# Kernel tuning notes

Hardware: AMD Instinct MI355X
Metric: run time of the kernel (lower is better)

The kernel has to match this reference:

```python
import jax, jax.numpy as jnp
import numpy as np

DIM = 384; HEADS = 6; POINTS = 4; LEVELS = 3; HID = 96
B = 2; D0 = 12; H0 = 12; W0 = 12
NMID = D0 * H0 * W0          # mid-level tokens
NTOK = 73 * NMID // 8        # total tokens across 3 scales


def _ln(x, w, b, eps=1e-6):
    m = x.mean(-1, keepdims=True)
    v = ((x - m) ** 2).mean(-1, keepdims=True)
    return (x - m) * jax.lax.rsqrt(v + eps) * w + b


def _make_ref(shapes):
    # matches get_reference_points: per-level normalized centers, stacked as (d, x, y)
    refs = []
    for (D_, H_, W_) in shapes:
        d = (jnp.arange(D_, dtype=jnp.float32) + 0.5) / D_
        y = (jnp.arange(H_, dtype=jnp.float32) + 0.5) / H_
        x = (jnp.arange(W_, dtype=jnp.float32) + 0.5) / W_
        dd, yy, xx = jnp.meshgrid(d, y, x, indexing='ij')
        refs.append(jnp.stack([dd.ravel(), xx.ravel(), yy.ravel()], -1))
    return jnp.concatenate(refs, 0)[None, :, None, :]  # [1, N, 1, 3]


def _sample_level(v, D_, H_, W_, loc):
    # v: [B,S,h,hd]; loc: [B,Nq,h,P,3] normalized (d,x,y); trilinear, zero padding,
    # align_corners=False semantics (pixel = norm*size - 0.5)
    Bq, Nq, h, P, _ = loc.shape
    hd = v.shape[-1]
    pd = loc[..., 0] * D_ - 0.5
    px = loc[..., 1] * W_ - 0.5
    py = loc[..., 2] * H_ - 0.5
    d0 = jnp.floor(pd); x0 = jnp.floor(px); y0 = jnp.floor(py)
    fd = pd - d0; fx = px - x0; fy = py - y0
    d0 = d0.astype(jnp.int32); x0 = x0.astype(jnp.int32); y0 = y0.astype(jnp.int32)
    acc = jnp.zeros((Bq, Nq, h, P, hd), v.dtype)
    for dd in (0, 1):  # fixed 8-corner loop
        for dy in (0, 1):
            for dx in (0, 1):
                di = d0 + dd; yi = y0 + dy; xi = x0 + dx
                wgt = (fd if dd else 1.0 - fd) * (fy if dy else 1.0 - fy) * (fx if dx else 1.0 - fx)
                valid = ((di >= 0) & (di < D_) & (yi >= 0) & (yi < H_) & (xi >= 0) & (xi < W_)).astype(v.dtype)
                idx = (jnp.clip(di, 0, D_ - 1) * H_ + jnp.clip(yi, 0, H_ - 1)) * W_ + jnp.clip(xi, 0, W_ - 1)
                idx_t = idx.transpose(0, 1, 3, 2).reshape(Bq, Nq * P, h)
                g = jnp.take_along_axis(v, idx_t[..., None], axis=1)  # [B,Nq*P,h,hd]
                g = g.reshape(Bq, Nq, P, h, hd).transpose(0, 1, 3, 2, 4)
                acc = acc + (wgt * valid)[..., None] * g
    return acc  # [B,Nq,h,P,hd]


def _msdeform(q, ref, feat, shapes, off_w, off_b, aw_w, aw_b, val_w, val_b, out_w, out_b):
    Bq, Nq, C = q.shape
    hd = C // HEADS
    value = (feat @ val_w + val_b).reshape(Bq, -1, HEADS, hd)
    off = (q @ off_w + off_b).reshape(Bq, Nq, HEADS, LEVELS, POINTS, 3)
    aw = jax.nn.softmax((q @ aw_w + aw_b).reshape(Bq, Nq, HEADS, LEVELS * POINTS), -1)
    aw = aw.reshape(Bq, Nq, HEADS, LEVELS, POINTS)
    # offset normalizer in (d, x, y) order -> (D, W, H)
    norm = jnp.array([[D_, W_, H_] for (D_, H_, W_) in shapes], dtype=q.dtype)
    loc = ref[:, :, None, :, None, :] + off / norm[None, None, None, :, None, :]
    out = jnp.zeros((Bq, Nq, HEADS, hd), q.dtype)
    start = 0
    for l, (D_, H_, W_) in enumerate(shapes):
        S = D_ * H_ * W_
        sampled = _sample_level(value[:, start:start + S], D_, H_, W_, loc[:, :, :, l])
        out = out + jnp.einsum('bqhp,bqhpd->bqhd', aw[:, :, :, l], sampled)
        start += S
    return out.reshape(Bq, Nq, C) @ out_w + out_b


def _dwconv_seg(x, Dv, Hv, Wv, w, b):
    Bq, S, C = x.shape
    xv = x.reshape(Bq, Dv, Hv, Wv, C)
    y = jax.lax.conv_general_dilated(xv, w, (1, 1, 1), 'SAME',
                                     dimension_numbers=('NDHWC', 'DHWIO', 'NDHWC'),
                                     feature_group_count=C) + b
    return y.reshape(Bq, S, C)


def _conv_ffn(x, D, H, W, fc1_w, fc1_b, dw_w, dw_b, fc2_w, fc2_b):
    x = x @ fc1_w + fc1_b
    n = x.shape[1] // 73
    x1 = _dwconv_seg(x[:, :64 * n], 2 * D, 2 * H, 2 * W, dw_w, dw_b)
    x2 = _dwconv_seg(x[:, 64 * n:72 * n], D, H, W, dw_w, dw_b)
    x3 = _dwconv_seg(x[:, 72 * n:], D // 2, H // 2, W // 2, dw_w, dw_b)
    x = jax.nn.gelu(jnp.concatenate([x1, x2, x3], 1), approximate=False)
    return x @ fc2_w + fc2_b


def _forward(query, feat, D, H, W,
             qnorm_w, qnorm_b, fnorm_w, fnorm_b, ext_qnorm_w, ext_qnorm_b,
             ext_fnorm_w, ext_fnorm_b, ffn_norm_w, ffn_norm_b,
             off_w, off_b, aw_w, aw_b, val_w, val_b, out_w, out_b,
             fc1_w, fc1_b, dw_w, dw_b, fc2_w, fc2_b):
    n_mid = D * H * W
    n_high = 8 * n_mid
    x2 = query[:, n_high:n_high + n_mid] + feat
    q = jnp.concatenate([query[:, :n_high], x2, query[:, n_high + n_mid:]], 1)
    shapes = [(2 * D, 2 * H, 2 * W), (D, H, W), (D // 2, H // 2, W // 2)]
    ref = _make_ref(shapes)
    qn = _ln(q, qnorm_w, qnorm_b)      # CTI_toC.query_norm
    fn = _ln(q, fnorm_w, fnorm_b)      # CTI_toC.feat_norm
    aq = _ln(qn, ext_qnorm_w, ext_qnorm_b)  # MultiscaleExtractor.query_norm
    af = _ln(fn, ext_fnorm_w, ext_fnorm_b)  # MultiscaleExtractor.feat_norm
    out = qn + _msdeform(aq, ref, af, shapes, off_w, off_b, aw_w, aw_b, val_w, val_b, out_w, out_b)
    out = out + _conv_ffn(_ln(out, ffn_norm_w, ffn_norm_b), D, H, W,
                          fc1_w, fc1_b, dw_w, dw_b, fc2_w, fc2_b)
    return out


def setup_inputs() -> dict:
    key = jax.random.key(0)
    ks = jax.random.split(key, 16)
    w = lambda k, *s: jax.random.normal(k, s, jnp.float32) * 0.02
    NO = HEADS * LEVELS * POINTS * 3
    NA = HEADS * LEVELS * POINTS
    return {
        'query': jax.random.normal(ks[0], (B, NTOK, DIM), jnp.float32),
        'reference_points': jax.random.uniform(ks[1], (1, NTOK, 1, 3), dtype=jnp.float32),
        'feat': jax.random.normal(ks[2], (B, NMID, DIM), jnp.float32),
        'spatial_shapes': jnp.array([[2 * D0, 2 * H0, 2 * W0], [D0, H0, W0], [D0 // 2, H0 // 2, W0 // 2]], jnp.int32),
        'level_start_index': jnp.array([0, 8 * NMID, 9 * NMID], jnp.int32),
        'D': D0, 'H': H0, 'W': W0,
        'qnorm_w': jnp.ones(DIM), 'qnorm_b': jnp.zeros(DIM),
        'fnorm_w': jnp.ones(DIM), 'fnorm_b': jnp.zeros(DIM),
        'ext_qnorm_w': jnp.ones(DIM), 'ext_qnorm_b': jnp.zeros(DIM),
        'ext_fnorm_w': jnp.ones(DIM), 'ext_fnorm_b': jnp.zeros(DIM),
        'ffn_norm_w': jnp.ones(DIM), 'ffn_norm_b': jnp.zeros(DIM),
        'off_w': w(ks[3], DIM, NO), 'off_b': jnp.zeros(NO),
        'aw_w': w(ks[4], DIM, NA), 'aw_b': jnp.zeros(NA),
        'val_w': w(ks[5], DIM, DIM), 'val_b': jnp.zeros(DIM),
        'out_w': w(ks[6], DIM, DIM), 'out_b': jnp.zeros(DIM),
        'fc1_w': w(ks[7], DIM, HID), 'fc1_b': jnp.zeros(HID),
        'dw_w': w(ks[8], 3, 3, 3, 1, HID), 'dw_b': jnp.zeros(HID),
        'fc2_w': w(ks[9], HID, DIM), 'fc2_b': jnp.zeros(DIM),
    }


def reference(query, reference_points, feat, spatial_shapes, level_start_index, D, H, W,
              qnorm_w, qnorm_b, fnorm_w, fnorm_b, ext_qnorm_w, ext_qnorm_b,
              ext_fnorm_w, ext_fnorm_b, ffn_norm_w, ffn_norm_b,
              off_w, off_b, aw_w, aw_b, val_w, val_b, out_w, out_b,
              fc1_w, fc1_b, dw_w, dw_b, fc2_w, fc2_b):
    # reference_points / spatial_shapes / level_start_index are required by the torch
    # signature but unused: CTI_toC recomputes deform inputs internally.
    return _forward(query, feat, D, H, W,
                    qnorm_w, qnorm_b, fnorm_w, fnorm_b, ext_qnorm_w, ext_qnorm_b,
                    ext_fnorm_w, ext_fnorm_b, ffn_norm_w, ffn_norm_b,
                    off_w, off_b, aw_w, aw_b, val_w, val_b, out_w, out_b,
                    fc1_w, fc1_b, dw_w, dw_b, fc2_w, fc2_b)
```

## Files before the change

kernel.cpp:

```cpp
#include <hip/hip_runtime.h>
#include <hip/hip_fp16.h>
#include <cstdint>
#include <cstddef>

#define DIM    384
#define HEADS  6
#define HD     64
#define NTOK   15768
#define NMID   1728
#define BATCH  2
#define ROWS   (BATCH*NTOK)
#define MPAD   31616
#define L1START 13824
#define L2START 15552
#define HID    96
#define VROWS  (ROWS + 8)
#define VSLAB  ((size_t)VROWS * 64)

typedef __attribute__((ext_vector_type(8))) short short8;
typedef __attribute__((ext_vector_type(4))) float floatx4;

__device__ __forceinline__ unsigned short f2bf(float x){
  unsigned u = __float_as_uint(x);
  unsigned r = (u + 0x7FFFu + ((u >> 16) & 1u)) >> 16;
  return (unsigned short)r;
}

__device__ __forceinline__ unsigned cvt_pk_bf16(float lo, float hi){
  unsigned r;
  asm("v_cvt_pk_bf16_f32 %0, %1, %2" : "=v"(r) : "v"(lo), "v"(hi));
  return r;
}

template<int C>
__device__ __forceinline__ int dpp_i(int v){
  return __builtin_amdgcn_mov_dpp(v, C, 0xF, 0xF, true);
}
template<int C>
__device__ __forceinline__ float dpp_f(float v){
  return __int_as_float(dpp_i<C>(__float_as_int(v)));
}
#define ROR8 0x128
#define ROR4 0x124
#define ROR2 0x122
#define ROR1 0x121

__device__ __forceinline__ __half2 h2_of(int v){ return *(__half2*)&v; }
__device__ __forceinline__ int i_of(__half2 v){ return *(int*)&v; }

__device__ __forceinline__ __half2 xor32_hadd(__half2 a){
  int x = i_of(a), y = x;
  asm volatile("v_permlane32_swap_b32 %0, %1" : "+v"(x), "+v"(y));
  return __hadd2(h2_of(x), h2_of(y));
}

__device__ __forceinline__ float wave_sum(float v){
  #pragma unroll
  for (int o = 32; o; o >>= 1) v += __shfl_xor(v, o, 64);
  return v;
}

__device__ __forceinline__ void ln384(const float* x, float* y,
                                      const float* __restrict__ w,
                                      const float* __restrict__ b, int lane){
  float s = 0.f;
  #pragma unroll
  for (int j = 0; j < 6; j++) s += x[j];
  s = wave_sum(s);
  float m = s * (1.f/384.f);
  float v = 0.f;
  #pragma unroll
  for (int j = 0; j < 6; j++){ float d = x[j] - m; v += d*d; }
  v = wave_sum(v) * (1.f/384.f);
  float rs = rsqrtf(v + 1e-6f);
  #pragma unroll
  for (int j = 0; j < 6; j++){
    int c = j*64 + lane;
    y[j] = (x[j] - m) * rs * w[c] + b[c];
  }
}

__global__ void k_ln_front(const float* __restrict__ query, const float* __restrict__ feat,
                           const float* __restrict__ qw,  const float* __restrict__ qb,
                           const float* __restrict__ fw,  const float* __restrict__ fb,
                           const float* __restrict__ eqw, const float* __restrict__ eqb,
                           const float* __restrict__ efw, const float* __restrict__ efb,
                           float* __restrict__ qn, unsigned short* __restrict__ aq,
                           unsigned short* __restrict__ af){
  int wid = blockIdx.x * (blockDim.x >> 6) + (threadIdx.x >> 6);
  if (wid >= ROWS) return;
  int lane = threadIdx.x & 63;
  int b = wid / NTOK, t = wid - b*NTOK;
  const float* qp = query + (size_t)wid * DIM;
  float x[6];
  #pragma unroll
  for (int j = 0; j < 6; j++) x[j] = qp[j*64 + lane];
  if (t >= L1START && t < L2START){
    const float* fp = feat + ((size_t)b*NMID + (t - L1START)) * DIM;
    #pragma unroll
    for (int j = 0; j < 6; j++) x[j] += fp[j*64 + lane];
  }
  float y[6], z[6];
  ln384(x, y, qw, qb, lane);
  {
    float* o = qn + (size_t)wid * DIM;
    #pragma unroll
    for (int j = 0; j < 6; j++) o[j*64 + lane] = y[j];
  }
  ln384(y, z, eqw, eqb, lane);
  {
    unsigned short* o = aq + (size_t)wid * DIM;
    #pragma unroll
    for (int j = 0; j < 6; j++) o[j*64 + lane] = f2bf(z[j]);
  }
  ln384(x, y, fw, fb, lane);
  ln384(y, z, efw, efb, lane);
  {
    unsigned short* o = af + (size_t)wid * DIM;
    #pragma unroll
    for (int j = 0; j < 6; j++) o[j*64 + lane] = f2bf(z[j]);
  }
}

__global__ void k_ln(const float* __restrict__ in, const float* __restrict__ w,
                     const float* __restrict__ b, unsigned short* __restrict__ out){
  int wid = blockIdx.x * (blockDim.x >> 6) + (threadIdx.x >> 6);
  if (wid >= ROWS) return;
  int lane = threadIdx.x & 63;
  float x[6], y[6];
  const float* p = in + (size_t)wid * DIM;
  #pragma unroll
  for (int j = 0; j < 6; j++) x[j] = p[j*64 + lane];
  ln384(x, y, w, b, lane);
  unsigned short* o = out + (size_t)wid * DIM;
  #pragma unroll
  for (int j = 0; j < 6; j++) o[j*64 + lane] = f2bf(y[j]);
}

__global__ void k_cvt_all(const float* __restrict__ val_w, const float* __restrict__ off_w,
                          const float* __restrict__ aw_w,  const float* __restrict__ out_w,
                          const float* __restrict__ fc1_w, const float* __restrict__ fc2_w,
                          const float* __restrict__ off_b, const float* __restrict__ aw_b,
                          unsigned short* __restrict__ wt_val, unsigned short* __restrict__ wt_offaw,
                          unsigned short* __restrict__ wt_out, unsigned short* __restrict__ wt_fc1,
                          unsigned short* __restrict__ wt_fc2, float* __restrict__ offaw_b,
                          unsigned short* __restrict__ vt_pad){
  int id = blockIdx.x * blockDim.x + threadIdx.x;
  if (id < 147456){
    int n = id / 384, k = id - n*384;
    wt_val[id] = f2bf(val_w[(size_t)k*384 + n]);
  } else if (id < 294912){
    int i = id - 147456;
    int n = i / 384, k = i - n*384;
    float v = 0.f;
    if (n < 216) v = off_w[(size_t)k*216 + n];
    else if (n >= 256 && n < 328) v = aw_w[(size_t)k*72 + (n-256)];
    wt_offaw[i] = f2bf(v);
  } else if (id < 442368){
    int i = id - 294912;
    int n = i / 384, k = i - n*384;
    wt_out[i] = f2bf(out_w[(size_t)k*384 + n]);
  } else if (id < 491520){
    int i = id - 442368;
    int n = i / 384, k = i - n*384;
    wt_fc1[i] = f2bf((n < 96) ? fc1_w[(size_t)k*96 + n] : 0.f);
  } else if (id < 528384){
    int i = id - 491520;
    int n = i / 96, k = i - n*96;
    wt_fc2[i] = f2bf(fc2_w[(size_t)k*384 + n]);
  } else if (id < 528768){
    int n = id - 528384;
    float v = 0.f;
    if (n < 216) v = off_b[n];
    else if (n >= 256 && n < 328) v = aw_b[n-256];
    offaw_b[n] = v;
  } else if (id < 531840){
    int i = id - 528768;
    int hh = i >> 9, rem = i & 511;
    vt_pad[(size_t)hh * VSLAB + (size_t)ROWS * 64 + rem] = 0;
  }
}

template<int OUTMODE>
__global__ __launch_bounds__(256) void k_gemm(
    const unsigned short* __restrict__ A,
    const unsigned short* __restrict__ Wt,
    const float* __restrict__ bias,
    const float* __restrict__ R,
    void* __restrict__ Cv,
    int M, int N, int K){
  __shared__ __align__(16) unsigned short As[2*128*32];
  __shared__ __align__(16) unsigned short Bs[2*128*32];
  int tid = threadIdx.x;
  int w = tid >> 6, lane = tid & 63;
  int m0 = blockIdx.y * 128, n0 = blockIdx.x * 128;
  int m_off = (w & 1) * 64, n_off = (w >> 1) * 64;

  floatx4 acc[4][4] = {};

  int sr = lane >> 2;
  int sc = (lane & 3) * 8;
  int lrow = lane & 15;
  int kq = (lane >> 4) * 8;

#define GSTAGE(BUF, K0) { \
    _Pragma("unroll") \
    for (int s2 = 0; s2 < 2; s2++){ \
      int c = w * 2 + s2; \
      const unsigned short* ga = A  + (size_t)(m0 + c*16 + sr) * K + (K0) + sc; \
      __builtin_amdgcn_global_load_lds( \
          (const __attribute__((address_space(1))) void*)ga, \
          (__attribute__((address_space(3))) void*)(As + (BUF)*4096 + c*512), 16, 0, 0); \
      const unsigned short* gb = Wt + (size_t)(n0 + c*16 + sr) * K + (K0) + sc; \
      __builtin_amdgcn_global_load_lds( \
          (const __attribute__((address_space(1))) void*)gb, \
          (__attribute__((address_space(3))) void*)(Bs + (BUF)*4096 + c*512), 16, 0, 0); \
    } }

  GSTAGE(0, 0)
  __syncthreads();

  int cur = 0;
  for (int k0 = 0; k0 < K; k0 += 32){
    if (k0 + 32 < K){ GSTAGE(cur ^ 1, k0 + 32) }
    const unsigned short* Ab = As + cur*4096;
    const unsigned short* Bb = Bs + cur*4096;
    short8 afr[4], bfr[4];
    #pragma unroll
    for (int i = 0; i < 4; i++)
      afr[i] = *(const short8*)(Ab + (m_off + i*16 + lrow)*32 + kq);
    #pragma unroll
    for (int j = 0; j < 4; j++)
      bfr[j] = *(const short8*)(Bb + (n_off + j*16 + lrow)*32 + kq);
    #pragma unroll
    for (int i = 0; i < 4; i++)
      #pragma unroll
      for (int j = 0; j < 4; j++)
        acc[i][j] = __builtin_amdgcn_mfma_f32_16x16x32_bf16(afr[i], bfr[j], acc[i][j], 0, 0, 0);
    __syncthreads();
    cur ^= 1;
  }
#undef GSTAGE

  int cn = n0 + n_off + lrow;
  int rbase = m0 + m_off + (lane >> 4) * 4;
  #pragma unroll
  for (int j = 0; j < 4; j++){
    int n = cn + j*16;
    if (n >= N) continue;
    float bj = bias[n];
    #pragma unroll
    for (int i = 0; i < 4; i++){
      int mb = rbase + i*16;
      #pragma unroll
      for (int r = 0; r < 4; r++){
        int m = mb + r;
        if (m < M){
          float v = acc[i][j][r] + bj;
          if (R) v += R[(size_t)m * N + n];
          if (OUTMODE == 0)      ((float*)Cv)[(size_t)m * N + n] = v;
          else if (OUTMODE == 3) ((__half*)Cv)[(size_t)m * N + n] = __float2half_rn(v);
          else {
            ((__half*)Cv)[(size_t)(n >> 6) * VSLAB + (size_t)m * 64 + (n & 63)] =
                __float2half_rn(v);
          }
        }
      }
    }
  }
}

__global__ __launch_bounds__(64, 4) void k_msdeform(const __half* __restrict__ vt,
                                                    const float* __restrict__ offaw,
                                                    unsigned short* __restrict__ msout){
  __shared__ __align__(16) int2 dsc[48];
  int bid = blockIdx.x;
  int seq = (bid & 7) * ((ROWS*HEADS)/8) + (bid >> 3);
  int head = seq / ROWS;
  int r = seq - head * ROWS;
  int lane = threadIdx.x & 63;
  int b = (r >= NTOK) ? 1 : 0;
  int t = r - b * NTOK;

  float refd, refy, refx;
  if (t < L1START){
    int i = t;
    int dd = i / 576; int rem = i - dd*576; int yy = rem / 24; int xx = rem - yy*24;
    refd = (dd + 0.5f) * (1.f/24.f); refy = (yy + 0.5f) * (1.f/24.f); refx = (xx + 0.5f) * (1.f/24.f);
  } else if (t < L2START){
    int i = t - L1START;
    int dd = i / 144; int rem = i - dd*144; int yy = rem / 12; int xx = rem - yy*12;
    refd = (dd + 0.5f) * (1.f/12.f); refy = (yy + 0.5f) * (1.f/12.f); refx = (xx + 0.5f) * (1.f/12.f);
  } else {
    int i = t - L2START;
    int dd = i / 36; int rem = i - dd*36; int yy = rem / 6; int xx = rem - yy*6;
    refd = (dd + 0.5f) * (1.f/6.f); refy = (yy + 0.5f) * (1.f/6.f); refx = (xx + 0.5f) * (1.f/6.f);
  }

  int s   = lane & 15;
  int grp = lane >> 4;

  float logit = (s < 12) ? offaw[(size_t)r * 384 + 256 + head * 12 + s] : -1e30f;
  float mx = logit;
  mx = fmaxf(mx, dpp_f<ROR8>(mx));
  mx = fmaxf(mx, dpp_f<ROR4>(mx));
  mx = fmaxf(mx, dpp_f<ROR2>(mx));
  mx = fmaxf(mx, dpp_f<ROR1>(mx));
  float e = (s < 12) ? __expf(logit - mx) : 0.f;
  float sum = e;
  sum += dpp_f<ROR8>(sum);
  sum += dpp_f<ROR4>(sum);
  sum += dpp_f<ROR2>(sum);
  sum += dpp_f<ROR1>(sum);
  float aww = e / sum;

  if (s < 12){
    int j = s;
    int l = j >> 2;
    int Dl  = (l == 0) ? 24 : ((l == 1) ? 12 : 6);
    int lst = (l == 0) ? 0  : ((l == 1) ? L1START : L2START);
    const float* op = offaw + (size_t)r * 384 + head * 36 + j * 3;
    float od = op[0], ox = op[1], oy = op[2];
    float fDl = (float)Dl;
    float pd = refd * fDl + od - 0.5f;
    float px = refx * fDl + ox - 0.5f;
    float py = refy * fDl + oy - 0.5f;
    float fld = floorf(pd), flx = floorf(px), fly = floorf(py);
    float fd = pd - fld, fx = px - flx, fy = py - fly;
    int d0 = (int)fld, x0 = (int)flx, y0 = (int)fly;
    int cz = grp >> 1, cy = grp & 1;
    int di = d0 + cz, yi = y0 + cy;
    bool vzy = (di >= 0) & (di < Dl) & (yi >= 0) & (yi < Dl);
    float wz = cz ? fd : 1.f - fd;
    float wy = cy ? fy : 1.f - fy;
    float wp = vzy ? (wz * aww) * wy : 0.f;
    int rs = min(max(x0, 0), Dl - 1);
    float wlo_x = (rs == x0) ? (1.f - fx) : ((rs == x0 + 1) ? fx : 0.f);
    float whi_x = ((rs == x0) && (x0 + 1 < Dl)) ? fx : 0.f;
    int dc = min(max(di, 0), Dl - 1);
    int yc = min(max(yi, 0), Dl - 1);
    int rowk = (b * NTOK + lst) + (dc * Dl + yc) * Dl + rs;
    __half2 wh = __floats2half2_rn(wp * wlo_x, wp * whi_x);
    dsc[grp * 12 + s] = make_int2(rowk, *(int*)&wh);
  }
  const uint4* dq = (const uint4*)dsc;
  uint4 dp0 = dq[grp*6+0], dp1 = dq[grp*6+1], dp2 = dq[grp*6+2];
  uint4 dp3 = dq[grp*6+3], dp4 = dq[grp*6+4], dp5 = dq[grp*6+5];

  const char* vbase = (const char*)(vt + (size_t)head * VSLAB);
  unsigned laneoff = (unsigned)(lane & 15) << 4;
  unsigned selperm = (lane & 8) ? 0x03020302u : 0x01000100u;

  int rw[12] = {(int)dp0.x,(int)dp0.z,(int)dp1.x,(int)dp1.z,(int)dp2.x,(int)dp2.z,
                (int)dp3.x,(int)dp3.z,(int)dp4.x,(int)dp4.z,(int)dp5.x,(int)dp5.z};
  unsigned wg[12] = {dp0.y,dp0.w,dp1.y,dp1.w,dp2.y,dp2.w,
                     dp3.y,dp3.w,dp4.y,dp4.w,dp5.y,dp5.w};

  uint4 vd[12];
  #pragma unroll
  for (int j = 0; j < 12; j++)
    vd[j] = *(const uint4*)(vbase + ((((unsigned)rw[j]) << 7) + laneoff));
  __builtin_amdgcn_sched_barrier(0);

  unsigned wsel[12];
  #pragma unroll
  for (int j = 0; j < 12; j++)
    wsel[j] = __builtin_amdgcn_perm(wg[j], wg[j], selperm);

  __half2 hz; *(int*)&hz = 0;
  __half2 a0 = hz, a1 = hz, a2 = hz, a3 = hz;
  #pragma unroll
  for (int j = 0; j < 12; j++){
    __half2 wh = *(__half2*)&wsel[j];
    uint4 v = vd[j];
    a0 = __hfma2(wh, *(__half2*)&v.x, a0);
    a1 = __hfma2(wh, *(__half2*)&v.y, a1);
    a2 = __hfma2(wh, *(__half2*)&v.z, a2);
    a3 = __hfma2(wh, *(__half2*)&v.w, a3);
  }

  a0 = __hadd2(a0, h2_of(dpp_i<ROR8>(i_of(a0))));
  a1 = __hadd2(a1, h2_of(dpp_i<ROR8>(i_of(a1))));
  a2 = __hadd2(a2, h2_of(dpp_i<ROR8>(i_of(a2))));
  a3 = __hadd2(a3, h2_of(dpp_i<ROR8>(i_of(a3))));
  {
    int t0 = __shfl_xor(i_of(a0), 16, 64); a0 = __hadd2(a0, h2_of(t0));
    int t1 = __shfl_xor(i_of(a1), 16, 64); a1 = __hadd2(a1, h2_of(t1));
    int t2 = __shfl_xor(i_of(a2), 16, 64); a2 = __hadd2(a2, h2_of(t2));
    int t3 = __shfl_xor(i_of(a3), 16, 64); a3 = __hadd2(a3, h2_of(t3));
  }
  a0 = xor32_hadd(a0);
  a1 = xor32_hadd(a1);
  a2 = xor32_hadd(a2);
  a3 = xor32_hadd(a3);

  if (lane < 8){
    float2 f0 = __half22float2(a0), f1 = __half22float2(a1);
    float2 f2 = __half22float2(a2), f3 = __half22float2(a3);
    uint4 pk;
    pk.x = cvt_pk_bf16(f0.x, f0.y);
    pk.y = cvt_pk_bf16(f1.x, f1.y);
    pk.z = cvt_pk_bf16(f2.x, f2.y);
    pk.w = cvt_pk_bf16(f3.x, f3.y);
    *(uint4*)(msout + (size_t)r * DIM + head * 64 + lane * 8) = pk;
  }
}

__global__ void k_dwconv_gelu(const __half* __restrict__ h, const float* __restrict__ dww,
                              const float* __restrict__ dwb, unsigned short* __restrict__ h2){
  int gid = blockIdx.x * blockDim.x + threadIdx.x;
  if (gid >= ROWS * 24) return;
  int c4 = gid % 24;
  int r = gid / 24;
  int c = c4 * 4;
  int b = (r >= NTOK) ? 1 : 0;
  int t = r - b * NTOK;
  int base, DL, i;
  if (t < L1START){ base = 0; DL = 24; i = t; }
  else if (t < L2START){ base = L1START; DL = 12; i = t - L1START; }
  else { base = L2START; DL = 6; i = t - L2START; }
  int dd, yy, xx;
  if (DL == 24){ dd = i / 576; int rem = i - dd*576; yy = rem / 24; xx = rem - yy*24; }
  else if (DL == 12){ dd = i / 144; int rem = i - dd*144; yy = rem / 12; xx = rem - yy*12; }
  else { dd = i / 36; int rem = i - dd*36; yy = rem / 6; xx = rem - yy*6; }
  float4 acc = {0.f, 0.f, 0.f, 0.f};
  #pragma unroll
  for (int kz = 0; kz < 3; kz++){
    int nd = dd + kz - 1; if (nd < 0 || nd >= DL) continue;
    #pragma unroll
    for (int ky = 0; ky < 3; ky++){
      int ny = yy + ky - 1; if (ny < 0 || ny >= DL) continue;
      #pragma unroll
      for (int kx = 0; kx < 3; kx++){
        int nx = xx + kx - 1; if (nx < 0 || nx >= DL) continue;
        int nt = base + (nd * DL + ny) * DL + nx;
        uint2 raw = *(const uint2*)(h + ((size_t)(b*NTOK + nt)) * HID + c);
        float2 h01 = __half22float2(h2_of((int)raw.x));
        float2 h23 = __half22float2(h2_of((int)raw.y));
        float4 wv = *(const float4*)(dww + (size_t)((kz*3 + ky)*3 + kx) * HID + c);
        acc.x += h01.x * wv.x; acc.y += h01.y * wv.y;
        acc.z += h23.x * wv.z; acc.w += h23.y * wv.w;
      }
    }
  }
  float4 bv = *(const float4*)(dwb + c);
  acc.x += bv.x; acc.y += bv.y; acc.z += bv.z; acc.w += bv.w;
  const float k = 0.70710678118654752440f;
  float g0 = 0.5f * acc.x * (1.f + erff(acc.x * k));
  float g1 = 0.5f * acc.y * (1.f + erff(acc.y * k));
  float g2 = 0.5f * acc.z * (1.f + erff(acc.z * k));
  float g3 = 0.5f * acc.w * (1.f + erff(acc.w * k));
  uint2 pk;
  pk.x = ((unsigned)f2bf(g1) << 16) | (unsigned)f2bf(g0);
  pk.y = ((unsigned)f2bf(g3) << 16) | (unsigned)f2bf(g2);
  *(uint2*)(h2 + (size_t)r * HID + c) = pk;
}

extern "C" void kernel_launch(void* const* d_in, const int* in_sizes, int n_in,
                              void* d_out, int out_size, void* d_ws, size_t ws_size,
                              hipStream_t stream){
  const float* query = (const float*)d_in[0];
  const float* feat  = (const float*)d_in[2];
  const float* qnw = (const float*)d_in[8],  *qnb = (const float*)d_in[9];
  const float* fnw = (const float*)d_in[10], *fnb = (const float*)d_in[11];
  const float* eqw = (const float*)d_in[12], *eqb = (const float*)d_in[13];
  const float* efw = (const float*)d_in[14], *efb = (const float*)d_in[15];
  const float* ffw = (const float*)d_in[16], *ffb = (const float*)d_in[17];
  const float* off_w = (const float*)d_in[18], *off_b = (const float*)d_in[19];
  const float* aw_w  = (const float*)d_in[20], *aw_b  = (const float*)d_in[21];
  const float* val_w = (const float*)d_in[22], *val_b = (const float*)d_in[23];
  const float* out_w = (const float*)d_in[24], *out_b = (const float*)d_in[25];
  const float* fc1_w = (const float*)d_in[26], *fc1_b = (const float*)d_in[27];
  const float* dw_w  = (const float*)d_in[28], *dw_b  = (const float*)d_in[29];
  const float* fc2_w = (const float*)d_in[30], *fc2_b = (const float*)d_in[31];
  float* out = (float*)d_out;

  char* p = (char*)d_ws;
  float* qn             = (float*)p;          p += (size_t)ROWS*384*4;
  unsigned short* aq    = (unsigned short*)p; p += (size_t)MPAD*384*2;
  unsigned short* af    = (unsigned short*)p; p += (size_t)MPAD*384*2;
  __half* value_t       = (__half*)p;         p += (size_t)HEADS*VSLAB*2;
  float* offaw          = (float*)p;          p += (size_t)ROWS*384*4;
  unsigned short* wt_val   = (unsigned short*)p; p += (size_t)384*384*2;
  unsigned short* wt_offaw = (unsigned short*)p; p += (size_t)384*384*2;
  unsigned short* wt_out   = (unsigned short*)p; p += (size_t)384*384*2;
  unsigned short* wt_fc1   = (unsigned short*)p; p += (size_t)128*384*2;
  unsigned short* wt_fc2   = (unsigned short*)p; p += (size_t)384*96*2;
  float* offaw_b           = (float*)p;          p += (size_t)384*4;
  unsigned short* t_buf  = aq;
  unsigned short* msout  = af;
  float* y1              = offaw;
  __half* h_buf          = value_t;
  unsigned short* h2_buf = (unsigned short*)qn;

  k_cvt_all<<<(531840 + 255)/256, 256, 0, stream>>>(val_w, off_w, aw_w, out_w, fc1_w, fc2_w,
                                                    off_b, aw_b,
                                                    wt_val, wt_offaw, wt_out, wt_fc1, wt_fc2,
                                                    offaw_b, (unsigned short*)value_t);

  int lnBlocks = ROWS / 4;
  k_ln_front<<<lnBlocks, 256, 0, stream>>>(query, feat, qnw, qnb, fnw, fnb,
                                           eqw, eqb, efw, efb, qn, aq, af);

  dim3 gN384(3, MPAD/128), gN128(1, MPAD/128);

  k_gemm<2><<<gN384, 256, 0, stream>>>(af, wt_val, val_b, nullptr, value_t, ROWS, 384, 384);
  k_gemm<0><<<gN384, 256, 0, stream>>>(aq, wt_offaw, offaw_b, nullptr, offaw, ROWS, 384, 384);
  k_msdeform<<<ROWS * HEADS, 64, 0, stream>>>(value_t, offaw, msout);
  k_gemm<0><<<gN384, 256, 0, stream>>>(msout, wt_out, out_b, qn, y1, ROWS, 384, 384);
  k_ln<<<lnBlocks, 256, 0, stream>>>(y1, ffw, ffb, t_buf);
  k_gemm<3><<<gN128, 256, 0, stream>>>(t_buf, wt_fc1, fc1_b, nullptr, h_buf, ROWS, 96, 384);
  k_dwconv_gelu<<<(ROWS * 24 + 255)/256, 256, 0, stream>>>(h_buf, dw_w, dw_b, h2_buf);
  k_gemm<0><<<gN384, 256, 0, stream>>>(h2_buf, wt_fc2, fc2_b, y1, out, ROWS, 384, 96);
}
```

Baseline: 485.8 us.

## Store intermediates in fp16 and batch value/offset GEMMs into one launch

Intermediate activations (qn residual, offset/attention logits, y1) are now stored as fp16 instead of fp32. This halves the memory traffic for writing and re-reading them in the GEMM epilogues, msdeform and LN kernels. The value and offset GEMMs are merged into one launch using blockIdx.z, which removes a launch and fills more of the device, and a sched_barrier in msdeform is dropped. The cost is lower precision: offsets feed the sampling positions and the residual path, so accuracy could suffer.

Result: no change. 476.3 us (-2.0%).

```diff
diff --git a/kernel.cpp b/kernel.cpp
--- a/kernel.cpp
+++ b/kernel.cpp
@@ -85,7 +85,7 @@
                            const float* __restrict__ fw,  const float* __restrict__ fb,
                            const float* __restrict__ eqw, const float* __restrict__ eqb,
                            const float* __restrict__ efw, const float* __restrict__ efb,
-                           float* __restrict__ qn, unsigned short* __restrict__ aq,
+                           __half* __restrict__ qn, unsigned short* __restrict__ aq,
                            unsigned short* __restrict__ af){
   int wid = blockIdx.x * (blockDim.x >> 6) + (threadIdx.x >> 6);
   if (wid >= ROWS) return;
@@ -103,9 +103,9 @@
   float y[6], z[6];
   ln384(x, y, qw, qb, lane);
   {
-    float* o = qn + (size_t)wid * DIM;
-    #pragma unroll
-    for (int j = 0; j < 6; j++) o[j*64 + lane] = y[j];
+    __half* o = qn + (size_t)wid * DIM;
+    #pragma unroll
+    for (int j = 0; j < 6; j++) o[j*64 + lane] = __float2half_rn(y[j]);
   }
   ln384(y, z, eqw, eqb, lane);
   {
@@ -122,15 +122,15 @@
   }
 }
 
-__global__ void k_ln(const float* __restrict__ in, const float* __restrict__ w,
+__global__ void k_ln(const __half* __restrict__ in, const float* __restrict__ w,
                      const float* __restrict__ b, unsigned short* __restrict__ out){
   int wid = blockIdx.x * (blockDim.x >> 6) + (threadIdx.x >> 6);
   if (wid >= ROWS) return;
   int lane = threadIdx.x & 63;
   float x[6], y[6];
-  const float* p = in + (size_t)wid * DIM;
-  #pragma unroll
-  for (int j = 0; j < 6; j++) x[j] = p[j*64 + lane];
+  const __half* p = in + (size_t)wid * DIM;
+  #pragma unroll
+  for (int j = 0; j < 6; j++) x[j] = __half2float(p[j*64 + lane]);
   ln384(x, y, w, b, lane);
   unsigned short* o = out + (size_t)wid * DIM;
   #pragma unroll
@@ -181,27 +181,41 @@
   }
 }
 
-template<int OUTMODE>
-__global__ __launch_bounds__(256) void k_gemm(
-    const unsigned short* __restrict__ A,
-    const unsigned short* __restrict__ Wt,
-    const float* __restrict__ bias,
-    const float* __restrict__ R,
-    void* __restrict__ Cv,
-    int M, int N, int K){
-  __shared__ __align__(16) unsigned short As[2*128*32];
-  __shared__ __align__(16) unsigned short Bs[2*128*32];
-  int tid = threadIdx.x;
-  int w = tid >> 6, lane = tid & 63;
-  int m0 = blockIdx.y * 128, n0 = blockIdx.x * 128;
-  int m_off = (w & 1) * 64, n_off = (w >> 1) * 64;
-
-  floatx4 acc[4][4] = {};
-
-  int sr = lane >> 2;
-  int sc = (lane & 3) * 8;
-  int lrow = lane & 15;
-  int kq = (lane >> 4) * 8;
+#define GEMM_BODY(A, Wt, K)                                                        \
+  __shared__ __align__(16) unsigned short As[2*128*32];                            \
+  __shared__ __align__(16) unsigned short Bs[2*128*32];                            \
+  int tid = threadIdx.x;                                                           \
+  int w = tid >> 6, lane = tid & 63;                                               \
+  int m0 = blockIdx.y * 128, n0 = blockIdx.x * 128;                                \
+  int m_off = (w & 1) * 64, n_off = (w >> 1) * 64;                                 \
+  floatx4 acc[4][4] = {};                                                          \
+  int sr = lane >> 2;                                                              \
+  int sc = (lane & 3) * 8;                                                         \
+  int lrow = lane & 15;                                                            \
+  int kq = (lane >> 4) * 8;                                                        \
+  GSTAGE(0, 0)                                                                     \
+  __syncthreads();                                                                 \
+  int cur = 0;                                                                     \
+  for (int k0 = 0; k0 < (K); k0 += 32){                                            \
+    if (k0 + 32 < (K)){ GSTAGE(cur ^ 1, k0 + 32) }                                 \
+    const unsigned short* Ab = As + cur*4096;                                      \
+    const unsigned short* Bb = Bs + cur*4096;                                      \
+    short8 afr[4], bfr[4];                                                         \
+    _Pragma("unroll")                                                              \
+    for (int i = 0; i < 4; i++)                                                    \
+      afr[i] = *(const short8*)(Ab + (m_off + i*16 + lrow)*32 + kq);               \
+    _Pragma("unroll")                                                              \
+    for (int j = 0; j < 4; j++)                                                    \
+      bfr[j] = *(const short8*)(Bb + (n_off + j*16 + lrow)*32 + kq);               \
+    _Pragma("unroll")                                                              \
+    for (int i = 0; i < 4; i++)                                                    \
+      _Pragma("unroll")                                                            \
+      for (int j = 0; j < 4; j++)                                                  \
+        acc[i][j] = __builtin_amdgcn_mfma_f32_16x16x32_bf16(afr[i], bfr[j],        \
+                                                            acc[i][j], 0, 0, 0);  \
+    __syncthreads();                                                               \
+    cur ^= 1;                                                                      \
+  }
 
 #define GSTAGE(BUF, K0) { \
     _Pragma("unroll") \
@@ -217,31 +231,15 @@
           (__attribute__((address_space(3))) void*)(Bs + (BUF)*4096 + c*512), 16, 0, 0); \
     } }
 
-  GSTAGE(0, 0)
-  __syncthreads();
-
-  int cur = 0;
-  for (int k0 = 0; k0 < K; k0 += 32){
-    if (k0 + 32 < K){ GSTAGE(cur ^ 1, k0 + 32) }
-    const unsigned short* Ab = As + cur*4096;
-    const unsigned short* Bb = Bs + cur*4096;
-    short8 afr[4], bfr[4];
-    #pragma unroll
-    for (int i = 0; i < 4; i++)
-      afr[i] = *(const short8*)(Ab + (m_off + i*16 + lrow)*32 + kq);
-    #pragma unroll
-    for (int j = 0; j < 4; j++)
-      bfr[j] = *(const short8*)(Bb + (n_off + j*16 + lrow)*32 + kq);
-    #pragma unroll
-    for (int i = 0; i < 4; i++)
-      #pragma unroll
-      for (int j = 0; j < 4; j++)
-        acc[i][j] = __builtin_amdgcn_mfma_f32_16x16x32_bf16(afr[i], bfr[j], acc[i][j], 0, 0, 0);
-    __syncthreads();
-    cur ^= 1;
-  }
-#undef GSTAGE
-
+template<int OUTMODE>
+__global__ __launch_bounds__(256) void k_gemm(
+    const unsigned short* __restrict__ A,
+    const unsigned short* __restrict__ Wt,
+    const float* __restrict__ bias,
+    const __half* __restrict__ R,
+    void* __restrict__ Cv,
+    int M, int N, int K){
+  GEMM_BODY(A, Wt, K)
   int cn = n0 + n_off + lrow;
   int rbase = m0 + m_off + (lane >> 4) * 4;
   #pragma unroll
@@ -257,21 +255,53 @@
         int m = mb + r;
         if (m < M){
           float v = acc[i][j][r] + bj;
-          if (R) v += R[(size_t)m * N + n];
-          if (OUTMODE == 0)      ((float*)Cv)[(size_t)m * N + n] = v;
-          else if (OUTMODE == 3) ((__half*)Cv)[(size_t)m * N + n] = __float2half_rn(v);
-          else {
-            ((__half*)Cv)[(size_t)(n >> 6) * VSLAB + (size_t)m * 64 + (n & 63)] =
-                __float2half_rn(v);
-          }
+          if (R) v += __half2float(R[(size_t)m * N + n]);
+          if (OUTMODE == 0) ((float*)Cv)[(size_t)m * N + n] = v;
+          else              ((__half*)Cv)[(size_t)m * N + n] = __float2half_rn(v);
         }
       }
     }
   }
 }
 
+__global__ __launch_bounds__(256) void k_gemm_pair(
+    const unsigned short* __restrict__ A0, const unsigned short* __restrict__ W0,
+    const float* __restrict__ b0, __half* __restrict__ C0,
+    const unsigned short* __restrict__ A1, const unsigned short* __restrict__ W1,
+    const float* __restrict__ b1, __half* __restrict__ C1,
+    int M, int N, int K){
+  int z = blockIdx.z;
+  const unsigned short* A  = z ? A1 : A0;
+  const unsigned short* Wt = z ? W1 : W0;
+  const float* bias = z ? b1 : b0;
+  GEMM_BODY(A, Wt, K)
+  int cn = n0 + n_off + lrow;
+  int rbase = m0 + m_off + (lane >> 4) * 4;
+  #pragma unroll
+  for (int j = 0; j < 4; j++){
+    int n = cn + j*16;
+    if (n >= N) continue;
+    float bj = bias[n];
+    #pragma unroll
+    for (int i = 0; i < 4; i++){
+      int mb = rbase + i*16;
+      #pragma unroll
+      for (int r = 0; r < 4; r++){
+        int m = mb + r;
+        if (m < M){
+          float v = acc[i][j][r] + bj;
+          if (z == 0)
+            C0[(size_t)(n >> 6) * VSLAB + (size_t)m * 64 + (n & 63)] = __float2half_rn(v);
+          else
+            C1[(size_t)m * N + n] = __float2half_rn(v);
+        }
+      }
+    }
+  }
+}
+
 __global__ __launch_bounds__(64, 4) void k_msdeform(const __half* __restrict__ vt,
-                                                    const float* __restrict__ offaw,
+                                                    const __half* __restrict__ offaw,
                                                     unsigned short* __restrict__ msout){
   __shared__ __align__(16) int2 dsc[48];
   int bid = blockIdx.x;
@@ -300,7 +330,7 @@
   int s   = lane & 15;
   int grp = lane >> 4;
 
-  float logit = (s < 12) ? offaw[(size_t)r * 384 + 256 + head * 12 + s] : -1e30f;
+  float logit = (s < 12) ? __half2float(offaw[(size_t)r * 384 + 256 + head * 12 + s]) : -1e30f;
   float mx = logit;
   mx = fmaxf(mx, dpp_f<ROR8>(mx));
   mx = fmaxf(mx, dpp_f<ROR4>(mx));
@@ -319,8 +349,8 @@
     int l = j >> 2;
     int Dl  = (l == 0) ? 24 : ((l == 1) ? 12 : 6);
     int lst = (l == 0) ? 0  : ((l == 1) ? L1START : L2START);
-    const float* op = offaw + (size_t)r * 384 + head * 36 + j * 3;
-    float od = op[0], ox = op[1], oy = op[2];
+    const __half* op = offaw + (size_t)r * 384 + head * 36 + j * 3;
+    float od = __half2float(op[0]), ox = __half2float(op[1]), oy = __half2float(op[2]);
     float fDl = (float)Dl;
     float pd = refd * fDl + od - 0.5f;
     float px = refx * fDl + ox - 0.5f;
@@ -360,8 +390,6 @@
   #pragma unroll
   for (int j = 0; j < 12; j++)
     vd[j] = *(const uint4*)(vbase + ((((unsigned)rw[j]) << 7) + laneoff));
-  __builtin_amdgcn_sched_barrier(0);
-
   unsigned wsel[12];
   #pragma unroll
   for (int j = 0; j < 12; j++)
@@ -476,11 +504,11 @@
   float* out = (float*)d_out;
 
   char* p = (char*)d_ws;
-  float* qn             = (float*)p;          p += (size_t)ROWS*384*4;
+  __half* qn            = (__half*)p;         p += (size_t)ROWS*384*2;
   unsigned short* aq    = (unsigned short*)p; p += (size_t)MPAD*384*2;
   unsigned short* af    = (unsigned short*)p; p += (size_t)MPAD*384*2;
   __half* value_t       = (__half*)p;         p += (size_t)HEADS*VSLAB*2;
-  float* offaw          = (float*)p;          p += (size_t)ROWS*384*4;
+  __half* offaw         = (__half*)p;         p += (size_t)ROWS*384*2;
   unsigned short* wt_val   = (unsigned short*)p; p += (size_t)384*384*2;
   unsigned short* wt_offaw = (unsigned short*)p; p += (size_t)384*384*2;
   unsigned short* wt_out   = (unsigned short*)p; p += (size_t)384*384*2;
@@ -489,7 +517,7 @@
   float* offaw_b           = (float*)p;          p += (size_t)384*4;
   unsigned short* t_buf  = aq;
   unsigned short* msout  = af;
-  float* y1              = offaw;
+  __half* y1             = offaw;
   __half* h_buf          = value_t;
   unsigned short* h2_buf = (unsigned short*)qn;
 
@@ -502,12 +530,13 @@
   k_ln_front<<<lnBlocks, 256, 0, stream>>>(query, feat, qnw, qnb, fnw, fnb,
                                            eqw, eqb, efw, efb, qn, aq, af);
 
-  dim3 gN384(3, MPAD/128), gN128(1, MPAD/128);
-
-  k_gemm<2><<<gN384, 256, 0, stream>>>(af, wt_val, val_b, nullptr, value_t, ROWS, 384, 384);
-  k_gemm<0><<<gN384, 256, 0, stream>>>(aq, wt_offaw, offaw_b, nullptr, offaw, ROWS, 384, 384);
+  dim3 gN384(3, MPAD/128), gN128(1, MPAD/128), gPair(3, MPAD/128, 2);
+
+  k_gemm_pair<<<gPair, 256, 0, stream>>>(af, wt_val, val_b, value_t,
+                                         aq, wt_offaw, offaw_b, offaw,
+                                         ROWS, 384, 384);
   k_msdeform<<<ROWS * HEADS, 64, 0, stream>>>(value_t, offaw, msout);
-  k_gemm<0><<<gN384, 256, 0, stream>>>(msout, wt_out, out_b, qn, y1, ROWS, 384, 384);
+  k_gemm<3><<<gN384, 256, 0, stream>>>(msout, wt_out, out_b, qn, y1, ROWS, 384, 384);
   k_ln<<<lnBlocks, 256, 0, stream>>>(y1, ffw, ffb, t_buf);
   k_gemm<3><<<gN128, 256, 0, stream>>>(t_buf, wt_fc1, fc1_b, nullptr, h_buf, ROWS, 96, 384);
   k_dwconv_gelu<<<(ROWS * 24 + 255)/256, 256, 0, stream>>>(h_buf, dw_w, dw_b, h2_buf);
```
